# Performance work log

Measured on AMD Instinct MI355X. Metric: run time of the kernel, lower is better.

## Reference

```python
import jax, jax.numpy as jnp
import numpy as np

B = 4096       # batch of query embeddings
E = 512        # embedding_size
C = 2000       # num_classes
PROXIES = 32   # imprinted weight vectors per class
P = C * PROXIES  # 64000 total stacked weight rows
EPS = 1e-12    # torch F.normalize eps


def _l2_normalize(x):
    # F.normalize(x, p=2, dim=1): divide by norm clamped to eps
    n = jnp.linalg.norm(x, axis=1, keepdims=True)
    return x / jnp.maximum(n, EPS)


def setup_inputs() -> dict:
    key = jax.random.key(0)
    k1, k2 = jax.random.split(key)
    data = jax.random.normal(k1, (B, E), dtype=jnp.float32)
    w1 = jax.random.normal(k2, (P, E), dtype=jnp.float32)
    segment_ids = jnp.arange(P, dtype=jnp.int32)  # raw row index; class id derived in reference
    return {"data": data, "w1": w1, "segment_ids": segment_ids}


def reference(data, w1, segment_ids):
    # class id of each stacked weight row (contiguous blocks, as torch vstack([*w1s]))
    seg = (segment_ids * C) // P  # == idx // PROXIES, shape [P]
    # normalize: input data at forward time; weights were l2-normalized at imprint time
    d = _l2_normalize(data)   # [B, E]
    w = _l2_normalize(w1)     # [P, E]
    # x = w1 @ data.T : per-proxy activations  [P, B]
    x = jnp.einsum('pe,be->pb', w, d)
    # per-class max over each class's ragged proxy block -> [C, B]
    y = jax.ops.segment_max(x, seg, num_segments=C)
    return y
```

## Files before the change

kernel.cpp:

```cpp
#include <hip/hip_runtime.h>

#define B_Q   4096
#define E_DIM 512
#define N_C   2000
#define N_P   64000

#define BM 128
#define BN 128

typedef int i32x4 __attribute__((ext_vector_type(4)));

__device__ __forceinline__ void async_ld16(const void* g, void* l) {
  __builtin_amdgcn_global_load_lds(
      (const __attribute__((address_space(1))) void*)g,
      (__attribute__((address_space(3))) void*)l,
      16, 0, 0);
}

__global__ __launch_bounds__(128) void normq_kernel(
    const float* __restrict__ w1, const float* __restrict__ data,
    signed char* __restrict__ wq, signed char* __restrict__ dq,
    float* __restrict__ wsc, float* __restrict__ dsc)
{
  int row = blockIdx.x;
  const float* in; signed char* outq; float* sc;
  if (row < N_P) { in = w1;   outq = wq; sc = wsc; }
  else           { in = data; outq = dq; sc = dsc; row -= N_P; }
  const int tid = threadIdx.x;
  const float4 v = *(const float4*)(in + (size_t)row * E_DIM + tid * 4);
  float ss = v.x*v.x + v.y*v.y + v.z*v.z + v.w*v.w;
  float am = fmaxf(fmaxf(fabsf(v.x), fabsf(v.y)), fmaxf(fabsf(v.z), fabsf(v.w)));
  #pragma unroll
  for (int s = 1; s < 64; s <<= 1) {
    ss += __shfl_xor(ss, s);
    am = fmaxf(am, __shfl_xor(am, s));
  }
  __shared__ float pss[2], pam[2];
  if ((tid & 63) == 0) { pss[tid >> 6] = ss; pam[tid >> 6] = am; }
  __syncthreads();
  const float inv = 1.0f / fmaxf(sqrtf(pss[0] + pss[1]), 1e-12f);
  const float m   = fmaxf(fmaxf(pam[0], pam[1]) * inv, 1e-20f);
  const float qs  = 127.0f / m * inv;
  char4 o;
  o.x = (signed char)__float2int_rn(v.x * qs);
  o.y = (signed char)__float2int_rn(v.y * qs);
  o.z = (signed char)__float2int_rn(v.z * qs);
  o.w = (signed char)__float2int_rn(v.w * qs);
  *(char4*)(outq + (size_t)row * E_DIM + tid * 4) = o;
  if (tid == 0) sc[row] = m * (1.0f / 127.0f);
}

#define WAITV(N) asm volatile("s_waitcnt vmcnt(" #N ")" ::: "memory")
#define LGKM0    asm volatile("s_waitcnt lgkmcnt(0)" ::: "memory")
#define SBAR     asm volatile("s_barrier" ::: "memory")
#define NOPS     do {} while (0)

#define STAGE_A(BUF,KOFF) do { \
  async_ld16(gA + (KOFF)*64,         smem + (BUF)*8192 + sdst); \
  async_ld16(gA + 32768 + (KOFF)*64, smem + (BUF)*8192 + sdst + 4096); \
} while(0)

#define STAGE_B(BUF,KOFF) do { \
  async_ld16(gB + (KOFF)*64,         smem + 16384 + (BUF)*8192 + sdst); \
  async_ld16(gB + 32768 + (KOFF)*64, smem + 16384 + (BUF)*8192 + sdst + 4096); \
} while(0)

#define RD(S,BUF) do { \
  fa##S##0 = *(const i32x4*)(pa + (BUF)*8192 +    0); \
  fa##S##1 = *(const i32x4*)(pa + (BUF)*8192 + 1024); \
  fa##S##2 = *(const i32x4*)(pa + (BUF)*8192 + 2048); \
  fa##S##3 = *(const i32x4*)(pa + (BUF)*8192 + 3072); \
  fb##S##0 = *(const i32x4*)(pb + (BUF)*8192 +    0); \
  fb##S##1 = *(const i32x4*)(pb + (BUF)*8192 + 1024); \
  fb##S##2 = *(const i32x4*)(pb + (BUF)*8192 + 2048); \
  fb##S##3 = *(const i32x4*)(pb + (BUF)*8192 + 3072); \
} while(0)

#define MM(S,m,n) \
  acc[m][n] = __builtin_amdgcn_mfma_i32_16x16x64_i8(fa##S##m, fb##S##n, acc[m][n], 0, 0, 0)

#define MFMA16(S) do { \
  MM(S,0,0); MM(S,0,1); MM(S,0,2); MM(S,0,3); \
  MM(S,1,0); MM(S,1,1); MM(S,1,2); MM(S,1,3); \
  MM(S,2,0); MM(S,2,1); MM(S,2,2); MM(S,2,3); \
  MM(S,3,0); MM(S,3,1); MM(S,3,2); MM(S,3,3); \
} while(0)

#define SGB(M,N) __builtin_amdgcn_sched_group_barrier(M, N, 0)
#define ILV8 do { \
  SGB(0x8,1); SGB(0x100,1); SGB(0x8,1); SGB(0x100,1); \
  SGB(0x8,1); SGB(0x100,1); SGB(0x8,1); SGB(0x100,1); \
  SGB(0x8,1); SGB(0x100,1); SGB(0x8,1); SGB(0x100,1); \
  SGB(0x8,1); SGB(0x100,1); SGB(0x8,1); SGB(0x100,1); \
  SGB(0x8,8); \
} while(0)

#define ITER(S,BUF, STAGE, WAIT, TAIL, ILV) do { \
  SBAR; \
  STAGE; \
  WAIT; \
  SBAR; \
  __builtin_amdgcn_sched_barrier(0); \
  __builtin_amdgcn_s_setprio(1); \
  MFMA16(S); \
  TAIL; \
  ILV; \
  LGKM0; \
  __builtin_amdgcn_s_setprio(0); \
} while(0)

__global__ __launch_bounds__(256, 3) void gemm_max_kernel(
    const signed char* __restrict__ wq,
    const signed char* __restrict__ dq,
    const float* __restrict__ wsc,
    const float* __restrict__ dsc,
    float* __restrict__ out)
{
  __shared__ __align__(16) char smem[32768];

  const int tid  = threadIdx.x;
  const int lane = tid & 63;
  const int wid  = tid >> 6;
  const int wr   = wid >> 1;
  const int wc   = wid & 1;

  const int bid  = blockIdx.x;
  const int wgid = (bid & 7) * 2000 + (bid >> 3);
  const int rowb = wgid >> 5;
  const int colb = wgid & 31;
  const int rowBase = rowb * BM;
  const int colBase = colb * BN;

  const int srow = tid >> 2;
  const int gch  = (tid & 3) ^ ((tid >> 3) & 3);
  const signed char* gA = wq + (size_t)(rowBase + srow) * E_DIM + gch * 16;
  const signed char* gB = dq + (size_t)(colBase + srow) * E_DIM + gch * 16;
  const int sdst = tid * 16;

  const int r   = lane & 15;
  const int kg  = lane >> 4;
  const int swz = (kg ^ ((r >> 1) & 3)) * 16;
  const char* pa = smem + (wr * 64 + r) * 64 + swz;
  const char* pb = smem + 16384 + (wc * 64 + r) * 64 + swz;

  i32x4 acc[4][4];
  #pragma unroll
  for (int m = 0; m < 4; ++m)
    #pragma unroll
    for (int n = 0; n < 4; ++n)
      acc[m][n] = (i32x4){0, 0, 0, 0};

  i32x4 fa00, fa01, fa02, fa03, fb00, fb01, fb02, fb03;
  i32x4 fa10, fa11, fa12, fa13, fb10, fb11, fb12, fb13;

  STAGE_A(0,0); STAGE_B(0,0);
  STAGE_A(1,1); STAGE_B(1,1);
  WAITV(4);
  SBAR;
  RD(0,0);
  LGKM0;

  ITER(0,0, STAGE_A(0,2); STAGE_B(0,2), WAITV(4), RD(1,1), ILV8);
  ITER(1,1, STAGE_A(1,3); STAGE_B(1,3), WAITV(4), RD(0,0), ILV8);
  ITER(0,0, STAGE_A(0,4); STAGE_B(0,4), WAITV(4), RD(1,1), ILV8);
  ITER(1,1, STAGE_A(1,5); STAGE_B(1,5), WAITV(4), RD(0,0), ILV8);
  ITER(0,0, STAGE_A(0,6); STAGE_B(0,6), WAITV(4), RD(1,1), ILV8);
  ITER(1,1, STAGE_A(1,7); STAGE_B(1,7), WAITV(4), RD(0,0), ILV8);
  ITER(0,0, NOPS,                       WAITV(0), RD(1,1), ILV8);
  ITER(1,1, NOPS,                       NOPS,     NOPS,    NOPS);

  float wsv[4][4];
  {
    #pragma unroll
    for (int m = 0; m < 4; ++m) {
      const float4 w4 = *(const float4*)(wsc + rowBase + wr * 64 + m * 16 + kg * 4);
      wsv[m][0] = w4.x; wsv[m][1] = w4.y; wsv[m][2] = w4.z; wsv[m][3] = w4.w;
    }
  }
  float dv[4];
  {
    const float* dscp = dsc + colBase + wc * 64 + r;
    #pragma unroll
    for (int n = 0; n < 4; ++n) dv[n] = dscp[n * 16];
  }
  const int classBase = rowb * 4 + wr * 2;
  #pragma unroll
  for (int q = 0; q < 2; ++q) {
    #pragma unroll
    for (int n = 0; n < 4; ++n) {
      float pm = -3.4e38f;
      #pragma unroll
      for (int j = 0; j < 4; ++j)
        pm = fmaxf(pm, fmaxf((float)acc[2*q][n][j]   * wsv[2*q][j],
                             (float)acc[2*q+1][n][j] * wsv[2*q+1][j]));
      pm = fmaxf(pm, __shfl_xor(pm, 16));
      pm = fmaxf(pm, __shfl_xor(pm, 32));
      if (lane < 16)
        out[(size_t)(classBase + q) * B_Q + colBase + wc * 64 + n * 16 + r]
            = pm * dv[n];
    }
  }
}

extern "C" void kernel_launch(void* const* d_in, const int* in_sizes, int n_in,
                              void* d_out, int out_size, void* d_ws, size_t ws_size,
                              hipStream_t stream) {
  const float* data = (const float*)d_in[0];
  const float* w1   = (const float*)d_in[1];
  float* out = (float*)d_out;

  signed char* wq = (signed char*)d_ws;
  signed char* dq = wq + (size_t)N_P * E_DIM;
  float* wsc = (float*)(dq + (size_t)B_Q * E_DIM);
  float* dsc = wsc + N_P;

  normq_kernel<<<N_P + B_Q, 128, 0, stream>>>(w1, data, wq, dq, wsc, dsc);
  gemm_max_kernel<<<(N_P / BM) * (B_Q / BN), 256, 0, stream>>>(wq, dq, wsc, dsc, out);
}
```

Measured before the change: 183.4 us.

## Load B operand fragments directly from global into registers, bypassing LDS

The data (B) operand is no longer staged through shared memory. Each wave now loads its own MFMA B fragments straight from global memory into registers, double-buffered one k-step ahead, while A keeps the async LDS path. This halves LDS use and LDS read traffic and could allow higher occupancy. In exchange, the two waves sharing a column now load the same B data twice from global/L2, and the vmcnt waits must now cover loads that go direct to registers as well as those going to LDS.

```diff
diff --git a/kernel.cpp b/kernel.cpp
--- a/kernel.cpp
+++ b/kernel.cpp
@@ -60,24 +60,22 @@
   async_ld16(gA + 32768 + (KOFF)*64, smem + (BUF)*8192 + sdst + 4096); \
 } while(0)
 
-#define STAGE_B(BUF,KOFF) do { \
-  async_ld16(gB + (KOFF)*64,         smem + 16384 + (BUF)*8192 + sdst); \
-  async_ld16(gB + 32768 + (KOFF)*64, smem + 16384 + (BUF)*8192 + sdst + 4096); \
-} while(0)
-
-#define RD(S,BUF) do { \
+#define LOADB(S,KT) do { \
+  gb##S##0 = *(const i32x4*)(gB0 + (KT)*64); \
+  gb##S##1 = *(const i32x4*)(gB1 + (KT)*64); \
+  gb##S##2 = *(const i32x4*)(gB2 + (KT)*64); \
+  gb##S##3 = *(const i32x4*)(gB3 + (KT)*64); \
+} while(0)
+
+#define RD_A(S,BUF) do { \
   fa##S##0 = *(const i32x4*)(pa + (BUF)*8192 +    0); \
   fa##S##1 = *(const i32x4*)(pa + (BUF)*8192 + 1024); \
   fa##S##2 = *(const i32x4*)(pa + (BUF)*8192 + 2048); \
   fa##S##3 = *(const i32x4*)(pa + (BUF)*8192 + 3072); \
-  fb##S##0 = *(const i32x4*)(pb + (BUF)*8192 +    0); \
-  fb##S##1 = *(const i32x4*)(pb + (BUF)*8192 + 1024); \
-  fb##S##2 = *(const i32x4*)(pb + (BUF)*8192 + 2048); \
-  fb##S##3 = *(const i32x4*)(pb + (BUF)*8192 + 3072); \
 } while(0)
 
 #define MM(S,m,n) \
-  acc[m][n] = __builtin_amdgcn_mfma_i32_16x16x64_i8(fa##S##m, fb##S##n, acc[m][n], 0, 0, 0)
+  acc[m][n] = __builtin_amdgcn_mfma_i32_16x16x64_i8(fa##S##m, gb##S##n, acc[m][n], 0, 0, 0)
 
 #define MFMA16(S) do { \
   MM(S,0,0); MM(S,0,1); MM(S,0,2); MM(S,0,3); \
@@ -87,17 +85,16 @@
 } while(0)
 
 #define SGB(M,N) __builtin_amdgcn_sched_group_barrier(M, N, 0)
-#define ILV8 do { \
-  SGB(0x8,1); SGB(0x100,1); SGB(0x8,1); SGB(0x100,1); \
-  SGB(0x8,1); SGB(0x100,1); SGB(0x8,1); SGB(0x100,1); \
-  SGB(0x8,1); SGB(0x100,1); SGB(0x8,1); SGB(0x100,1); \
-  SGB(0x8,1); SGB(0x100,1); SGB(0x8,1); SGB(0x100,1); \
+#define ILV4 do { \
+  SGB(0x8,2); SGB(0x100,1); SGB(0x8,2); SGB(0x100,1); \
+  SGB(0x8,2); SGB(0x100,1); SGB(0x8,2); SGB(0x100,1); \
   SGB(0x8,8); \
 } while(0)
 
-#define ITER(S,BUF, STAGE, WAIT, TAIL, ILV) do { \
+#define ITER(S, STAGEA, LDB, WAIT, TAIL, ILV) do { \
   SBAR; \
-  STAGE; \
+  STAGEA; \
+  LDB; \
   WAIT; \
   SBAR; \
   __builtin_amdgcn_sched_barrier(0); \
@@ -116,7 +113,7 @@
     const float* __restrict__ dsc,
     float* __restrict__ out)
 {
-  __shared__ __align__(16) char smem[32768];
+  __shared__ __align__(16) char smem[16384];
 
   const int tid  = threadIdx.x;
   const int lane = tid & 63;
@@ -134,14 +131,18 @@
   const int srow = tid >> 2;
   const int gch  = (tid & 3) ^ ((tid >> 3) & 3);
   const signed char* gA = wq + (size_t)(rowBase + srow) * E_DIM + gch * 16;
-  const signed char* gB = dq + (size_t)(colBase + srow) * E_DIM + gch * 16;
   const int sdst = tid * 16;
 
   const int r   = lane & 15;
   const int kg  = lane >> 4;
   const int swz = (kg ^ ((r >> 1) & 3)) * 16;
   const char* pa = smem + (wr * 64 + r) * 64 + swz;
-  const char* pb = smem + 16384 + (wc * 64 + r) * 64 + swz;
+
+  const signed char* gBb = dq + (size_t)(colBase + wc * 64 + r) * E_DIM + kg * 16;
+  const signed char* gB0 = gBb;
+  const signed char* gB1 = gBb + 16 * E_DIM;
+  const signed char* gB2 = gBb + 32 * E_DIM;
+  const signed char* gB3 = gBb + 48 * E_DIM;
 
   i32x4 acc[4][4];
   #pragma unroll
@@ -150,24 +151,25 @@
     for (int n = 0; n < 4; ++n)
       acc[m][n] = (i32x4){0, 0, 0, 0};
 
-  i32x4 fa00, fa01, fa02, fa03, fb00, fb01, fb02, fb03;
-  i32x4 fa10, fa11, fa12, fa13, fb10, fb11, fb12, fb13;
-
-  STAGE_A(0,0); STAGE_B(0,0);
-  STAGE_A(1,1); STAGE_B(1,1);
+  i32x4 fa00, fa01, fa02, fa03, fa10, fa11, fa12, fa13;
+  i32x4 gb00, gb01, gb02, gb03, gb10, gb11, gb12, gb13;
+
+  STAGE_A(0,0);
+  STAGE_A(1,1);
+  LOADB(0,0);
   WAITV(4);
   SBAR;
-  RD(0,0);
+  RD_A(0,0);
   LGKM0;
 
-  ITER(0,0, STAGE_A(0,2); STAGE_B(0,2), WAITV(4), RD(1,1), ILV8);
-  ITER(1,1, STAGE_A(1,3); STAGE_B(1,3), WAITV(4), RD(0,0), ILV8);
-  ITER(0,0, STAGE_A(0,4); STAGE_B(0,4), WAITV(4), RD(1,1), ILV8);
-  ITER(1,1, STAGE_A(1,5); STAGE_B(1,5), WAITV(4), RD(0,0), ILV8);
-  ITER(0,0, STAGE_A(0,6); STAGE_B(0,6), WAITV(4), RD(1,1), ILV8);
-  ITER(1,1, STAGE_A(1,7); STAGE_B(1,7), WAITV(4), RD(0,0), ILV8);
-  ITER(0,0, NOPS,                       WAITV(0), RD(1,1), ILV8);
-  ITER(1,1, NOPS,                       NOPS,     NOPS,    NOPS);
+  ITER(0, STAGE_A(0,2), LOADB(1,1), WAITV(6), RD_A(1,1), ILV4);
+  ITER(1, STAGE_A(1,3), LOADB(0,2), WAITV(6), RD_A(0,0), ILV4);
+  ITER(0, STAGE_A(0,4), LOADB(1,3), WAITV(6), RD_A(1,1), ILV4);
+  ITER(1, STAGE_A(1,5), LOADB(0,4), WAITV(6), RD_A(0,0), ILV4);
+  ITER(0, STAGE_A(0,6), LOADB(1,5), WAITV(6), RD_A(1,1), ILV4);
+  ITER(1, STAGE_A(1,7), LOADB(0,6), WAITV(6), RD_A(0,0), ILV4);
+  ITER(0, NOPS,         LOADB(1,7), WAITV(4), RD_A(1,1), ILV4);
+  ITER(1, NOPS,         NOPS,       WAITV(0), NOPS,      NOPS);
 
   float wsv[4][4];
   {
```

Result: slower. 294.9 us (median of 2 runs) (+60.8%).
